# Performance work log

Measured on AMD Instinct MI355X. Metric: run time of the kernel, lower is better.

## Reference

```python
import jax, jax.numpy as jnp
import numpy as np

N, E = 100000, 1600000
IN, HID, OUT, HEADS = 128, 128, 64, 4
HD = HID // HEADS  # per-head dim = 32


def setup_inputs() -> dict:
    key = jax.random.key(0)
    ks = jax.random.split(key, 16)
    p = lambda k, shape: (jax.random.normal(k, shape, jnp.float32) * 0.1)
    return {
        "x": jax.random.normal(ks[0], (N, IN), jnp.float32),
        "edge_index": jax.random.randint(ks[1], (2, E), 0, N, dtype=jnp.int32),
        # layer 0: GATConv(IN -> HD per head, HEADS heads)
        "W0": p(ks[2], (IN, HID)), "b0": jnp.zeros((HID,), jnp.float32),
        "as0": p(ks[3], (HEADS, HD)), "ad0": p(ks[4], (HEADS, HD)),
        # layer 1: GATConv(HID -> HD per head, HEADS heads)
        "W1": p(ks[5], (HID, HID)), "b1": jnp.zeros((HID,), jnp.float32),
        "as1": p(ks[6], (HEADS, HD)), "ad1": p(ks[7], (HEADS, HD)),
        # layer 2: GATConv(HID -> OUT, 1 head)
        "W2": p(ks[8], (HID, OUT)), "b2": jnp.zeros((OUT,), jnp.float32),
        "as2": p(ks[9], (1, OUT)), "ad2": p(ks[10], (1, OUT)),
    }


def _gat_conv(x, W, b, a_src, a_dst, src, dst, heads):
    """PyG GATConv forward (shared src/dst projection, self-loops pre-added)."""
    n = x.shape[0]
    h = (x @ W).reshape(n, heads, -1)                    # [N, H, C]
    al_s = jnp.sum(h * a_src, axis=-1)                   # [N, H]
    al_d = jnp.sum(h * a_dst, axis=-1)                   # [N, H]
    e = jax.nn.leaky_relu(al_s[src] + al_d[dst], 0.2)    # [Etot, H]
    # softmax over incoming edges of each destination node
    m = jax.ops.segment_max(e, dst, num_segments=n)
    p = jnp.exp(e - m[dst])
    s = jax.ops.segment_sum(p, dst, num_segments=n)
    alpha = p / (s[dst] + 1e-16)                         # PyG softmax eps
    out = jax.ops.segment_sum(h[src] * alpha[:, :, None], dst, num_segments=n)
    return out.reshape(n, -1) + b


def _l1norm(x):
    # F.normalize(x, p=1.0): dim=1, eps=1e-12
    return x / jnp.maximum(jnp.sum(jnp.abs(x), axis=1, keepdims=True), 1e-12)


def reference(x, edge_index, W0, b0, as0, ad0, W1, b1, as1, ad1, W2, b2, as2, ad2):
    n = x.shape[0]
    loop = jnp.arange(n, dtype=edge_index.dtype)
    src = jnp.concatenate([edge_index[0], loop])  # GATConv add_self_loops=True
    dst = jnp.concatenate([edge_index[1], loop])
    # layer 0 (dropout=identity in eval; layernorm output is dead code in source)
    h = _gat_conv(x, W0, b0, as0, ad0, src, dst, HEADS)
    h = _l1norm(jax.nn.leaky_relu(h, 0.01))
    # layer 1 (residual + layernorm results are overwritten in source -> dead)
    h = _gat_conv(h, W1, b1, as1, ad1, src, dst, HEADS)
    h = jax.nn.leaky_relu(h, 0.01)
    # layer 2 (single head)
    h = _gat_conv(h, W2, b2, as2, ad2, src, dst, 1)
    return jax.nn.relu(_l1norm(h))
```

## Files before the change

### kernel.cpp

```cpp
#include <hip/hip_runtime.h>
#include <hip/hip_bf16.h>

#define NN 100000
#define NE 1600000
#define NB 391
#define CHUNK 4096

typedef short bf8v __attribute__((ext_vector_type(8)));
typedef float f32x4 __attribute__((ext_vector_type(4)));

static __device__ __forceinline__ float lrelu(float x, float s) {
    return x > 0.f ? x : s * x;
}

static __device__ __forceinline__ unsigned short f2b(float f) {
    __hip_bfloat16 b = __float2bfloat16(f);
    return *reinterpret_cast<unsigned short*>(&b);
}

static __device__ __forceinline__ float blo(unsigned u) {
    return __uint_as_float(u << 16);
}
static __device__ __forceinline__ float bhi(unsigned u) {
    return __uint_as_float(u & 0xFFFF0000u);
}

struct alignas(4) bh2 {
    __hip_bfloat16 x, y;
};


__global__ __launch_bounds__(256) void bucket_hist(const int* __restrict__ dsts,
                                                   int* __restrict__ bcnt) {
    __shared__ int hist[NB];
    for (int t = threadIdx.x; t < NB; t += 256) hist[t] = 0;
    __syncthreads();
    int stride = gridDim.x * 256;
    for (int e = blockIdx.x * 256 + threadIdx.x; e < NE; e += stride)
        atomicAdd(&hist[dsts[e] >> 8], 1);
    __syncthreads();
    for (int t = threadIdx.x; t < NB; t += 256) {
        int c = hist[t];
        if (c) atomicAdd(&bcnt[t], c);
    }
}

__global__ __launch_bounds__(512) void bucket_scan(const int* __restrict__ bcnt,
                                                   int* __restrict__ bbase,
                                                   int* __restrict__ bcursor) {
    __shared__ int sd[512];
    int t = threadIdx.x;
    int v = (t < NB) ? bcnt[t] : 0;
    sd[t] = v;
    __syncthreads();
    for (int off = 1; off < 512; off <<= 1) {
        int x = (t >= off) ? sd[t - off] : 0;
        __syncthreads();
        sd[t] += x;
        __syncthreads();
    }
    int excl = sd[t] - v;
    if (t < NB) {
        bbase[t] = excl;
        bcursor[t] = excl;
    }
    if (t == NB - 1) bbase[NB] = excl + v;
}

__global__ __launch_bounds__(256) void partition_kernel(const int* __restrict__ srcs,
                                                        const int* __restrict__ dsts,
                                                        int* bcursor,
                                                        unsigned* __restrict__ part) {
    __shared__ int hist[NB];
    __shared__ int lbase[NB];
    for (int t = threadIdx.x; t < NB; t += 256) hist[t] = 0;
    __syncthreads();
    int e0 = blockIdx.x * CHUNK;
#pragma unroll
    for (int k = 0; k < CHUNK / 256; k++) {
        int e = e0 + k * 256 + threadIdx.x;
        if (e < NE) atomicAdd(&hist[dsts[e] >> 8], 1);
    }
    __syncthreads();
    for (int t = threadIdx.x; t < NB; t += 256) {
        int c = hist[t];
        if (c) lbase[t] = atomicAdd(&bcursor[t], c);
        hist[t] = 0;
    }
    __syncthreads();
#pragma unroll
    for (int k = 0; k < CHUNK / 256; k++) {
        int e = e0 + k * 256 + threadIdx.x;
        if (e < NE) {
            int s = srcs[e], d = dsts[e];
            int b = d >> 8;
            int r = atomicAdd(&hist[b], 1);
            part[lbase[b] + r] = (((unsigned)d & 255u) << 24) | (unsigned)s;
        }
    }
}

__global__ __launch_bounds__(256) void bucket_fill(const unsigned* __restrict__ part,
                                                   const int* __restrict__ bbase,
                                                   int* __restrict__ offs,
                                                   int* __restrict__ csr) {
    __shared__ int lcur[256];
    __shared__ int sd[256];
    int b = blockIdx.x;
    int t = threadIdx.x;
    int ebeg = bbase[b], eend = bbase[b + 1];
    int node0 = b << 8;
    int nNodes = min(256, NN - node0);
    lcur[t] = 0;
    __syncthreads();
    for (int e = ebeg + t; e < eend; e += 256) {
        unsigned p = part[e];
        atomicAdd(&lcur[p >> 24], 1);
    }
    __syncthreads();
    int cnt = lcur[t];
    sd[t] = cnt;
    __syncthreads();
    for (int off = 1; off < 256; off <<= 1) {
        int x = (t >= off) ? sd[t - off] : 0;
        __syncthreads();
        sd[t] += x;
        __syncthreads();
    }
    int start = ebeg + sd[t] - cnt;
    if (t < nNodes) offs[node0 + t] = start;
    if (b == NB - 1 && t == 0) offs[NN] = NE;
    lcur[t] = start;
    __syncthreads();
    for (int e = ebeg + t; e < eend; e += 256) {
        unsigned p = part[e];
        int pos = atomicAdd(&lcur[p >> 24], 1);
        csr[pos] = (int)(p & 0xFFFFFFu);
    }
}


template <int NOUT, int HEADS, bool AF32>
__global__ __launch_bounds__(256) void gemm_fused(
    const float* __restrict__ A32, const unsigned short* __restrict__ A16,
    const float* __restrict__ W, const float* __restrict__ asrc,
    const float* __restrict__ adst, unsigned short* __restrict__ h16out,
    float* __restrict__ als, float* __restrict__ ald, int n) {
    constexpr int NF = NOUT / 16;
    constexpr int PITCH = 136;
    __shared__ unsigned short Wl[NOUT * PITCH];

    const int tid = threadIdx.x;
    for (int i = tid; i < (128 * NOUT) / 4; i += 256) {
        int idx = i * 4;
        int k = idx / NOUT;
        int c = idx - k * NOUT;
        float4 wv = *(const float4*)&W[idx];
        Wl[(c + 0) * PITCH + k] = f2b(wv.x);
        Wl[(c + 1) * PITCH + k] = f2b(wv.y);
        Wl[(c + 2) * PITCH + k] = f2b(wv.z);
        Wl[(c + 3) * PITCH + k] = f2b(wv.w);
    }
    __syncthreads();

    const int lane = tid & 63, wave = tid >> 6;
    const int c = lane & 15, hi = lane >> 4;
    const int r0 = blockIdx.x * 64;
    const int arow = min(r0 + wave * 16 + c, n - 1);
    const int kb = hi * 8;

    f32x4 acc[NF];
#pragma unroll
    for (int nf = 0; nf < NF; ++nf) acc[nf] = 0;

#pragma unroll
    for (int kc = 0; kc < 4; ++kc) {
        bf8v a;
        if constexpr (AF32) {
            const float* ap = A32 + (size_t)arow * 128 + kc * 32 + kb;
            float4 f0 = *(const float4*)ap;
            float4 f1 = *(const float4*)(ap + 4);
            union {
                bf8v v;
                unsigned short u[8];
            } ua;
            ua.u[0] = f2b(f0.x);
            ua.u[1] = f2b(f0.y);
            ua.u[2] = f2b(f0.z);
            ua.u[3] = f2b(f0.w);
            ua.u[4] = f2b(f1.x);
            ua.u[5] = f2b(f1.y);
            ua.u[6] = f2b(f1.z);
            ua.u[7] = f2b(f1.w);
            a = ua.v;
        } else {
            a = *(const bf8v*)(A16 + (size_t)arow * 128 + kc * 32 + kb);
        }
#pragma unroll
        for (int nf = 0; nf < NF; ++nf) {
            bf8v b = *(const bf8v*)&Wl[(nf * 16 + c) * PITCH + kc * 32 + kb];
            acc[nf] = __builtin_amdgcn_mfma_f32_16x16x32_bf16(a, b, acc[nf], 0, 0, 0);
        }
    }

    float aS[NF], aD[NF];
#pragma unroll
    for (int nf = 0; nf < NF; ++nf) {
        aS[nf] = asrc[nf * 16 + c];
        aD[nf] = adst[nf * 16 + c];
    }
    float sRes[HEADS][4], dRes[HEADS][4];
#pragma unroll
    for (int hh = 0; hh < HEADS; ++hh) {
#pragma unroll
        for (int reg = 0; reg < 4; ++reg) {
            float s = 0.f, d = 0.f;
#pragma unroll
            for (int nf = hh * (NF / HEADS); nf < (hh + 1) * (NF / HEADS); ++nf) {
                s += acc[nf][reg] * aS[nf];
                d += acc[nf][reg] * aD[nf];
            }
#pragma unroll
            for (int o = 1; o < 16; o <<= 1) {
                s += __shfl_xor(s, o);
                d += __shfl_xor(d, o);
            }
            sRes[hh][reg] = s;
            dRes[hh][reg] = d;
        }
    }
    if (c == 0) {
#pragma unroll
        for (int reg = 0; reg < 4; ++reg) {
            int ro = r0 + wave * 16 + hi * 4 + reg;
            if (ro < n) {
                if constexpr (HEADS == 4) {
                    *(float4*)&als[ro * 4] =
                        make_float4(sRes[0][reg], sRes[1][reg], sRes[2][reg], sRes[3][reg]);
                    *(float4*)&ald[ro * 4] =
                        make_float4(dRes[0][reg], dRes[1][reg], dRes[2][reg], dRes[3][reg]);
                } else {
                    als[ro] = sRes[0][reg];
                    ald[ro] = dRes[0][reg];
                }
            }
        }
    }

    __syncthreads();
#pragma unroll
    for (int nf = 0; nf < NF; ++nf) {
#pragma unroll
        for (int reg = 0; reg < 4; ++reg) {
            int rl = wave * 16 + hi * 4 + reg;
            Wl[rl * PITCH + nf * 16 + c] = f2b(acc[nf][reg]);
        }
    }
    __syncthreads();
    constexpr int SEGS = NOUT / 8;
    for (int i = tid; i < 64 * SEGS; i += 256) {
        int rl = i / SEGS, sg = i - rl * SEGS;
        int ro = r0 + rl;
        if (ro < n)
            *(uint4*)&h16out[(size_t)ro * NOUT + sg * 8] =
                *(const uint4*)&Wl[rl * PITCH + sg * 8];
    }
}


__global__ __launch_bounds__(256) void agg4_kernel(
    const char* __restrict__ hb, const float* __restrict__ als, const float* __restrict__ ald,
    const int* __restrict__ offs, const int* __restrict__ cur, const int* __restrict__ csr,
    const float* __restrict__ bias, __hip_bfloat16* __restrict__ out, int n, int do_l1) {
    __shared__ int soff[4][64];
    __shared__ float sp[4][64][4];
    int w = threadIdx.x >> 6;
    int v = blockIdx.x * 4 + w;
    if (v >= n) return;
    int lane = threadIdx.x & 63;
    int hd = lane >> 4;
    int lane4 = lane << 2;

    float4 av = *(const float4*)&ald[v * 4];
    float4 svv = *(const float4*)&als[v * 4];
    int begin = offs[v], end = cur[v];

    float ps0 = __expf(lrelu(svv.x + av.x, 0.2f));
    float ps1 = __expf(lrelu(svv.y + av.y, 0.2f));
    float ps2 = __expf(lrelu(svv.z + av.z, 0.2f));
    float ps3 = __expf(lrelu(svv.w + av.w, 0.2f));
    float psel = hd == 0 ? ps0 : hd == 1 ? ps1 : hd == 2 ? ps2 : ps3;
    unsigned uv = *(const unsigned*)(hb + (size_t)v * 256 + lane4);
    float acc0 = psel * blo(uv);
    float acc1 = psel * bhi(uv);
    float s0 = 0.f, s1 = 0.f, s2 = 0.f, s3 = 0.f;

    for (int base = begin; base < end; base += 64) {
        int idx = base + lane;
        int cnt = min(64, end - base);
        if (idx < end) {
            int s = csr[idx];
            float4 q = *(const float4*)&als[s * 4];
            float p0 = __expf(lrelu(q.x + av.x, 0.2f));
            float p1 = __expf(lrelu(q.y + av.y, 0.2f));
            float p2 = __expf(lrelu(q.z + av.z, 0.2f));
            float p3 = __expf(lrelu(q.w + av.w, 0.2f));
            soff[w][lane] = s << 8;
            sp[w][lane][0] = p0;
            sp[w][lane][1] = p1;
            sp[w][lane][2] = p2;
            sp[w][lane][3] = p3;
            s0 += p0; s1 += p1; s2 += p2; s3 += p3;
        }
        asm volatile("s_waitcnt lgkmcnt(0)" ::: "memory");
        int t = 0;
        for (; t + 8 <= cnt; t += 8) {
            int o0 = soff[w][t + 0], o1 = soff[w][t + 1];
            int o2 = soff[w][t + 2], o3 = soff[w][t + 3];
            int o4 = soff[w][t + 4], o5 = soff[w][t + 5];
            int o6 = soff[w][t + 6], o7 = soff[w][t + 7];
            float p0 = sp[w][t + 0][hd], p1 = sp[w][t + 1][hd];
            float p2 = sp[w][t + 2][hd], p3 = sp[w][t + 3][hd];
            float p4 = sp[w][t + 4][hd], p5 = sp[w][t + 5][hd];
            float p6 = sp[w][t + 6][hd], p7 = sp[w][t + 7][hd];
            unsigned u0 = *(const unsigned*)(hb + o0 + lane4);
            unsigned u1 = *(const unsigned*)(hb + o1 + lane4);
            unsigned u2 = *(const unsigned*)(hb + o2 + lane4);
            unsigned u3 = *(const unsigned*)(hb + o3 + lane4);
            unsigned u4 = *(const unsigned*)(hb + o4 + lane4);
            unsigned u5 = *(const unsigned*)(hb + o5 + lane4);
            unsigned u6 = *(const unsigned*)(hb + o6 + lane4);
            unsigned u7 = *(const unsigned*)(hb + o7 + lane4);
            acc0 += p0 * blo(u0);
            acc1 += p0 * bhi(u0);
            acc0 += p1 * blo(u1);
            acc1 += p1 * bhi(u1);
            acc0 += p2 * blo(u2);
            acc1 += p2 * bhi(u2);
            acc0 += p3 * blo(u3);
            acc1 += p3 * bhi(u3);
            acc0 += p4 * blo(u4);
            acc1 += p4 * bhi(u4);
            acc0 += p5 * blo(u5);
            acc1 += p5 * bhi(u5);
            acc0 += p6 * blo(u6);
            acc1 += p6 * bhi(u6);
            acc0 += p7 * blo(u7);
            acc1 += p7 * bhi(u7);
        }
        for (; t < cnt; ++t) {
            int oa = soff[w][t];
            float pa = sp[w][t][hd];
            unsigned ua = *(const unsigned*)(hb + oa + lane4);
            acc0 += pa * blo(ua);
            acc1 += pa * bhi(ua);
        }
    }
#pragma unroll
    for (int o = 32; o > 0; o >>= 1) {
        s0 += __shfl_xor(s0, o);
        s1 += __shfl_xor(s1, o);
        s2 += __shfl_xor(s2, o);
        s3 += __shfl_xor(s3, o);
    }
    s0 += ps0; s1 += ps1; s2 += ps2; s3 += ps3;
    float ssel = hd == 0 ? s0 : hd == 1 ? s1 : hd == 2 ? s2 : s3;
    float inv = 1.f / (ssel + 1e-16f);
    float2 bv = *(const float2*)&bias[2 * lane];
    float o0 = lrelu(acc0 * inv + bv.x, 0.01f);
    float o1 = lrelu(acc1 * inv + bv.y, 0.01f);
    if (do_l1) {
        float t = fabsf(o0) + fabsf(o1);
#pragma unroll
        for (int o = 32; o > 0; o >>= 1) t += __shfl_xor(t, o);
        float li = 1.f / fmaxf(t, 1e-12f);
        o0 *= li;
        o1 *= li;
    }
    bh2 pk;
    pk.x = __float2bfloat16(o0);
    pk.y = __float2bfloat16(o1);
    *(bh2*)&out[(size_t)v * 128 + 2 * lane] = pk;
}


__global__ __launch_bounds__(256) void agg1_kernel(
    const char* __restrict__ hb, const float* __restrict__ als, const float* __restrict__ ald,
    const int* __restrict__ offs, const int* __restrict__ cur, const int* __restrict__ csr,
    const float* __restrict__ bias, float* __restrict__ out, int n) {
    __shared__ int soff[4][64];
    __shared__ float sp[4][64];
    int w = threadIdx.x >> 6;
    int v = blockIdx.x * 4 + w;
    if (v >= n) return;
    int lane = threadIdx.x & 63;
    int lane2 = lane << 1;
    float aldv = ald[v];
    float alsv = als[v];
    int begin = offs[v], end = cur[v];

    float pself = __expf(lrelu(alsv + aldv, 0.2f));
    unsigned short usv = *(const unsigned short*)(hb + (size_t)v * 128 + lane2);
    float acc = pself * __uint_as_float(((unsigned)usv) << 16);
    float ssum = 0.f;

    for (int base = begin; base < end; base += 64) {
        int idx = base + lane;
        int cnt = min(64, end - base);
        if (idx < end) {
            int s = csr[idx];
            float p = __expf(lrelu(als[s] + aldv, 0.2f));
            soff[w][lane] = s << 7;
            sp[w][lane] = p;
            ssum += p;
        }
        asm volatile("s_waitcnt lgkmcnt(0)" ::: "memory");
        int t = 0;
        for (; t + 8 <= cnt; t += 8) {
            int o0 = soff[w][t + 0], o1 = soff[w][t + 1];
            int o2 = soff[w][t + 2], o3 = soff[w][t + 3];
            int o4 = soff[w][t + 4], o5 = soff[w][t + 5];
            int o6 = soff[w][t + 6], o7 = soff[w][t + 7];
            float p0 = sp[w][t + 0], p1 = sp[w][t + 1];
            float p2 = sp[w][t + 2], p3 = sp[w][t + 3];
            float p4 = sp[w][t + 4], p5 = sp[w][t + 5];
            float p6 = sp[w][t + 6], p7 = sp[w][t + 7];
            unsigned short u0 = *(const unsigned short*)(hb + o0 + lane2);
            unsigned short u1 = *(const unsigned short*)(hb + o1 + lane2);
            unsigned short u2 = *(const unsigned short*)(hb + o2 + lane2);
            unsigned short u3 = *(const unsigned short*)(hb + o3 + lane2);
            unsigned short u4 = *(const unsigned short*)(hb + o4 + lane2);
            unsigned short u5 = *(const unsigned short*)(hb + o5 + lane2);
            unsigned short u6 = *(const unsigned short*)(hb + o6 + lane2);
            unsigned short u7 = *(const unsigned short*)(hb + o7 + lane2);
            acc += p0 * __uint_as_float(((unsigned)u0) << 16);
            acc += p1 * __uint_as_float(((unsigned)u1) << 16);
            acc += p2 * __uint_as_float(((unsigned)u2) << 16);
            acc += p3 * __uint_as_float(((unsigned)u3) << 16);
            acc += p4 * __uint_as_float(((unsigned)u4) << 16);
            acc += p5 * __uint_as_float(((unsigned)u5) << 16);
            acc += p6 * __uint_as_float(((unsigned)u6) << 16);
            acc += p7 * __uint_as_float(((unsigned)u7) << 16);
        }
        for (; t < cnt; ++t) {
            int oa = soff[w][t];
            float pa = sp[w][t];
            unsigned short ua = *(const unsigned short*)(hb + oa + lane2);
            acc += pa * __uint_as_float(((unsigned)ua) << 16);
        }
    }
#pragma unroll
    for (int o = 32; o > 0; o >>= 1) ssum += __shfl_xor(ssum, o);
    ssum += pself;
    float o = acc / (ssum + 1e-16f) + bias[lane];
    float t = fabsf(o);
#pragma unroll
    for (int off = 32; off > 0; off >>= 1) t += __shfl_xor(t, off);
    o = o / fmaxf(t, 1e-12f);
    out[(size_t)v * 64 + lane] = fmaxf(o, 0.f);
}


extern "C" void kernel_launch(void* const* d_in, const int* in_sizes, int n_in,
                              void* d_out, int out_size, void* d_ws, size_t ws_size,
                              hipStream_t stream) {
    const float* x = (const float*)d_in[0];
    const int* ei = (const int*)d_in[1];
    const float* W0 = (const float*)d_in[2];
    const float* b0 = (const float*)d_in[3];
    const float* as0 = (const float*)d_in[4];
    const float* ad0 = (const float*)d_in[5];
    const float* W1 = (const float*)d_in[6];
    const float* b1 = (const float*)d_in[7];
    const float* as1 = (const float*)d_in[8];
    const float* ad1 = (const float*)d_in[9];
    const float* W2 = (const float*)d_in[10];
    const float* b2 = (const float*)d_in[11];
    const float* as2 = (const float*)d_in[12];
    const float* ad2 = (const float*)d_in[13];
    float* outp = (float*)d_out;

    char* ws = (char*)d_ws;
    size_t off = 0;
    auto alloc = [&](size_t bytes) -> void* {
        void* p = ws + off;
        off = (off + bytes + 255) & ~(size_t)255;
        return p;
    };
    int* offs = (int*)alloc((NN + 1) * 4);
    int* bcnt = (int*)alloc(NB * 4);
    int* bbase = (int*)alloc((NB + 1) * 4);
    int* bcursor = (int*)alloc(NB * 4);
    unsigned* part = (unsigned*)alloc((size_t)NE * 4);
    int* csr = (int*)alloc((size_t)NE * 4);
    unsigned short* h16 = (unsigned short*)alloc((size_t)NN * 128 * 2);
    unsigned short* a16 = (unsigned short*)alloc((size_t)NN * 128 * 2);
    float* als = (float*)alloc(NN * 4 * 4);
    float* ald = (float*)alloc(NN * 4 * 4);

    const int* srcs = ei;
    const int* dsts = ei + NE;

    hipMemsetAsync(bcnt, 0, NB * 4, stream);
    bucket_hist<<<NB, 256, 0, stream>>>(dsts, bcnt);
    bucket_scan<<<1, 512, 0, stream>>>(bcnt, bbase, bcursor);
    partition_kernel<<<(NE + CHUNK - 1) / CHUNK, 256, 0, stream>>>(srcs, dsts, bcursor, part);
    bucket_fill<<<NB, 256, 0, stream>>>(part, bbase, offs, csr);

    int ggrid = (NN + 63) / 64;
    int aggrid = (NN + 3) / 4;

    gemm_fused<128, 4, true><<<ggrid, 256, 0, stream>>>(x, nullptr, W0, as0, ad0, h16, als, ald,
                                                        NN);
    agg4_kernel<<<aggrid, 256, 0, stream>>>((const char*)h16, als, ald, offs, offs + 1, csr, b0,
                                            (__hip_bfloat16*)a16, NN, 1);
    gemm_fused<128, 4, false><<<ggrid, 256, 0, stream>>>(nullptr, a16, W1, as1, ad1, h16, als,
                                                         ald, NN);
    agg4_kernel<<<aggrid, 256, 0, stream>>>((const char*)h16, als, ald, offs, offs + 1, csr, b1,
                                            (__hip_bfloat16*)a16, NN, 0);
    gemm_fused<64, 1, false><<<ggrid, 256, 0, stream>>>(nullptr, a16, W2, as2, ad2, h16, als,
                                                        ald, NN);
    agg1_kernel<<<aggrid, 256, 0, stream>>>((const char*)h16, als, ald, offs, offs + 1, csr, b2,
                                            outp, NN);
}
```

Before: 380.3 us.

## Replace global-atomic bucket partition with per-block histogram matrix and scan

The edge bucketing pipeline now records a per-block, per-bucket histogram matrix. A single-block scan turns it into exclusive offsets, so the scatter kernel needs no global atomics and no second histogram pass over dsts. This also drops the memset and the separate global histogram kernel. In exchange, the scan kernel runs a serial 391-step loop per thread over the matrix in one block, which could be slow.

Measured after the change: 387.4 us. Within noise of the previous version (+1.9%).

```diff
diff --git a/kernel.cpp b/kernel.cpp
--- a/kernel.cpp
+++ b/kernel.cpp
@@ -5,6 +5,7 @@
 #define NE 1600000
 #define NB 391
 #define CHUNK 4096
+#define NBLK 391
 
 typedef short bf8v __attribute__((ext_vector_type(8)));
 typedef float f32x4 __attribute__((ext_vector_type(4)));
@@ -30,28 +31,35 @@
 };
 
 
-__global__ __launch_bounds__(256) void bucket_hist(const int* __restrict__ dsts,
-                                                   int* __restrict__ bcnt) {
+__global__ __launch_bounds__(256) void csr_count(const int* __restrict__ dsts,
+                                                 int* __restrict__ histmat) {
     __shared__ int hist[NB];
     for (int t = threadIdx.x; t < NB; t += 256) hist[t] = 0;
     __syncthreads();
-    int stride = gridDim.x * 256;
-    for (int e = blockIdx.x * 256 + threadIdx.x; e < NE; e += stride)
-        atomicAdd(&hist[dsts[e] >> 8], 1);
-    __syncthreads();
-    for (int t = threadIdx.x; t < NB; t += 256) {
-        int c = hist[t];
-        if (c) atomicAdd(&bcnt[t], c);
-    }
-}
-
-__global__ __launch_bounds__(512) void bucket_scan(const int* __restrict__ bcnt,
-                                                   int* __restrict__ bbase,
-                                                   int* __restrict__ bcursor) {
+    int e0 = blockIdx.x * CHUNK;
+#pragma unroll
+    for (int k = 0; k < CHUNK / 256; k++) {
+        int e = e0 + k * 256 + threadIdx.x;
+        if (e < NE) atomicAdd(&hist[dsts[e] >> 8], 1);
+    }
+    __syncthreads();
+    for (int t = threadIdx.x; t < NB; t += 256) histmat[blockIdx.x * NB + t] = hist[t];
+}
+
+__global__ __launch_bounds__(512) void csr_scan(int* __restrict__ histmat,
+                                                int* __restrict__ bbase) {
     __shared__ int sd[512];
     int t = threadIdx.x;
-    int v = (t < NB) ? bcnt[t] : 0;
-    sd[t] = v;
+    int run = 0;
+    if (t < NB) {
+        for (int blk = 0; blk < NBLK; ++blk) {
+            int idx = blk * NB + t;
+            int v = histmat[idx];
+            histmat[idx] = run;
+            run += v;
+        }
+    }
+    sd[t] = run;
     __syncthreads();
     for (int off = 1; off < 512; off <<= 1) {
         int x = (t >= off) ? sd[t - off] : 0;
@@ -59,43 +67,29 @@
         sd[t] += x;
         __syncthreads();
     }
-    int excl = sd[t] - v;
-    if (t < NB) {
-        bbase[t] = excl;
-        bcursor[t] = excl;
-    }
-    if (t == NB - 1) bbase[NB] = excl + v;
-}
-
-__global__ __launch_bounds__(256) void partition_kernel(const int* __restrict__ srcs,
-                                                        const int* __restrict__ dsts,
-                                                        int* bcursor,
-                                                        unsigned* __restrict__ part) {
-    __shared__ int hist[NB];
-    __shared__ int lbase[NB];
-    for (int t = threadIdx.x; t < NB; t += 256) hist[t] = 0;
-    __syncthreads();
-    int e0 = blockIdx.x * CHUNK;
-#pragma unroll
-    for (int k = 0; k < CHUNK / 256; k++) {
-        int e = e0 + k * 256 + threadIdx.x;
-        if (e < NE) atomicAdd(&hist[dsts[e] >> 8], 1);
-    }
-    __syncthreads();
-    for (int t = threadIdx.x; t < NB; t += 256) {
-        int c = hist[t];
-        if (c) lbase[t] = atomicAdd(&bcursor[t], c);
-        hist[t] = 0;
-    }
-    __syncthreads();
+    int excl = sd[t] - run;
+    if (t < NB) bbase[t] = excl;
+    if (t == NB - 1) bbase[NB] = excl + run;
+}
+
+__global__ __launch_bounds__(256) void csr_scatter(const int* __restrict__ srcs,
+                                                   const int* __restrict__ dsts,
+                                                   const int* __restrict__ histmat,
+                                                   const int* __restrict__ bbase,
+                                                   unsigned* __restrict__ part) {
+    __shared__ int cur[NB];
+    int blk = blockIdx.x;
+    for (int t = threadIdx.x; t < NB; t += 256)
+        cur[t] = bbase[t] + histmat[blk * NB + t];
+    __syncthreads();
+    int e0 = blk * CHUNK;
 #pragma unroll
     for (int k = 0; k < CHUNK / 256; k++) {
         int e = e0 + k * 256 + threadIdx.x;
         if (e < NE) {
             int s = srcs[e], d = dsts[e];
-            int b = d >> 8;
-            int r = atomicAdd(&hist[b], 1);
-            part[lbase[b] + r] = (((unsigned)d & 255u) << 24) | (unsigned)s;
+            int r = atomicAdd(&cur[d >> 8], 1);
+            part[r] = (((unsigned)d & 255u) << 24) | (unsigned)s;
         }
     }
 }
@@ -488,9 +482,8 @@
         return p;
     };
     int* offs = (int*)alloc((NN + 1) * 4);
-    int* bcnt = (int*)alloc(NB * 4);
+    int* histmat = (int*)alloc((size_t)NBLK * NB * 4);
     int* bbase = (int*)alloc((NB + 1) * 4);
-    int* bcursor = (int*)alloc(NB * 4);
     unsigned* part = (unsigned*)alloc((size_t)NE * 4);
     int* csr = (int*)alloc((size_t)NE * 4);
     unsigned short* h16 = (unsigned short*)alloc((size_t)NN * 128 * 2);
@@ -501,10 +494,9 @@
     const int* srcs = ei;
     const int* dsts = ei + NE;
 
-    hipMemsetAsync(bcnt, 0, NB * 4, stream);
-    bucket_hist<<<NB, 256, 0, stream>>>(dsts, bcnt);
-    bucket_scan<<<1, 512, 0, stream>>>(bcnt, bbase, bcursor);
-    partition_kernel<<<(NE + CHUNK - 1) / CHUNK, 256, 0, stream>>>(srcs, dsts, bcursor, part);
+    csr_count<<<NBLK, 256, 0, stream>>>(dsts, histmat);
+    csr_scan<<<1, 512, 0, stream>>>(histmat, bbase);
+    csr_scatter<<<NBLK, 256, 0, stream>>>(srcs, dsts, histmat, bbase, part);
     bucket_fill<<<NB, 256, 0, stream>>>(part, bbase, offs, csr);
 
     int ggrid = (NN + 63) / 64;
```
